# Kernel optimization log

Measured on AMD Instinct MI355X. Metric: run time of the kernel, lower is better.

Reference implementation:

```python
import jax, jax.numpy as jnp
import numpy as np

B, T, D = 8, 2048, 256
EPS_NORM = 1e-8
EPS_LN = 1e-6


def _layer_norm(x, gamma, beta):
    mu = jnp.mean(x, axis=-1, keepdims=True)
    var = jnp.var(x, axis=-1, keepdims=True)
    return (x - mu) * jax.lax.rsqrt(var + EPS_LN) * gamma + beta


def setup_inputs() -> dict:
    key = jax.random.key(0)
    ks = jax.random.split(key, 8)
    xav = np.sqrt(2.0 / (D + D)).astype(np.float32)  # xavier_uniform-ish scale
    a_fea = jax.random.normal(ks[0], (B, T, D), jnp.float32)
    v_fea = jax.random.normal(ks[1], (B, T, D), jnp.float32)
    Wv1 = jax.random.normal(ks[2], (D, D), jnp.float32) * xav
    Wv2 = jax.random.normal(ks[3], (D, D), jnp.float32) * xav
    Wa1 = jax.random.normal(ks[4], (D, D), jnp.float32) * xav
    Wa2 = jax.random.normal(ks[5], (D, D), jnp.float32) * xav
    ln_gamma = jnp.ones((D,), jnp.float32)
    ln_beta = jnp.zeros((D,), jnp.float32)
    thr_val = jnp.asarray(0.099, jnp.float32)
    return {"a_fea": a_fea, "v_fea": v_fea, "Wv1": Wv1, "Wv2": Wv2,
            "Wa1": Wa1, "Wa2": Wa2, "ln_gamma": ln_gamma, "ln_beta": ln_beta,
            "thr_val": thr_val}


def reference(a_fea, v_fea, Wv1, Wv2, Wa1, Wa2, ln_gamma, ln_beta, thr_val):
    # Dropout is identity in eval mode. Linear(bias=False): x @ W^T; here W is [in, out].
    v_b1 = jax.nn.relu(jnp.einsum('btd,dh->bth', v_fea, Wv1))
    v_b2 = jax.nn.relu(jnp.einsum('btd,dh->bth', v_fea, Wv2))
    a_b1 = jax.nn.relu(jnp.einsum('btd,dh->bth', a_fea, Wa1))
    a_b2 = jax.nn.relu(jnp.einsum('btd,dh->bth', a_fea, Wa2))

    scale = 1.0 / jnp.sqrt(jnp.asarray(v_b2.shape[2], jnp.float32))
    # relu-gated cross-modal scores [B, Tv, Ta]
    beta = jax.nn.relu(jnp.einsum('bvh,bah->bva', v_b2, a_b1) * scale)

    # v->a: normalize over audio axis, threshold-sparsify
    beta_va = beta / (jnp.sum(beta, axis=-1, keepdims=True) + EPS_NORM)
    gamma_va = jnp.where(beta_va > thr_val, beta_va, 0.0)
    # a->v: transpose of UN-normalized beta (faithful to source ordering)
    beta_av = jnp.swapaxes(beta, 1, 2)
    beta_av = beta_av / (jnp.sum(beta_av, axis=-1, keepdims=True) + EPS_NORM)
    gamma_av = jnp.where(beta_av > thr_val, beta_av, 0.0)

    a_pos = jnp.einsum('bva,bah->bvh', gamma_va, a_b2)
    v_pos = jnp.einsum('bav,bvh->bah', gamma_av, v_b1)

    v_psp = _layer_norm(v_fea + a_pos, ln_gamma, ln_beta)
    a_psp = _layer_norm(a_fea + v_pos, ln_gamma, ln_beta)
    return (v_psp + a_psp) * 0.5
```

## Files before the change

kernel.cpp:

```cpp
#include <hip/hip_runtime.h>
#include <stdint.h>

#define B_ 8
#define T_ 2048
#define D_ 256
#define M_ (B_*T_)

typedef uint16_t u16;
typedef __attribute__((ext_vector_type(8))) short   short8;
typedef __attribute__((ext_vector_type(8))) __bf16  bf16x8;
typedef __attribute__((ext_vector_type(4))) float   f32x4;

__device__ __forceinline__ float bf2f(u16 b){
    union { uint32_t u; float f; } v; v.u = ((uint32_t)b) << 16; return v.f;
}
__device__ __forceinline__ u16 f2bf(float f){
    union { float f; uint32_t u; } v; v.f = f;
    uint32_t u = v.u;
    u += 0x7FFFu + ((u >> 16) & 1u);
    return (u16)(u >> 16);
}

__global__ void k_detect(const uint32_t* g, int* flag){
    *flag = (g[0] == 0x3F803F80u) ? 0 : 1;
}

struct WtArgs { const void* w[4]; u16* wt[4]; const int* flag; };

__global__ __launch_bounds__(256) void k_wt(WtArgs a){
    int f32in = *a.flag;
    int m = blockIdx.y;
    int d = blockIdx.x;
    int h = threadIdx.x;
    float val;
    if (f32in) val = ((const float*)a.w[m])[(size_t)d * D_ + h];
    else       val = bf2f(((const u16*)a.w[m])[(size_t)d * D_ + h]);
    a.wt[m][(size_t)h * D_ + d] = f2bf(val);
}

struct ProjArgs { const void* x[4]; const u16* wt[4]; u16* y[4]; u16* yt[4]; const int* flag; };

__global__ __launch_bounds__(256) void k_proj(ProjArgs args){
    __shared__ __align__(16) u16 Xs[128][72];
    __shared__ __align__(16) u16 Ws[128][72];
    int f32in = *args.flag;
    int id = blockIdx.x;
    int m  = id & 127;
    int vh = id >> 7;
    int hh = vh & 1;
    int v  = vh >> 1;
    const u16* Wt = args.wt[v];
    u16*       Y  = args.y[v];
    u16*       YT = args.yt[v];
    int t_base = m * 128;
    int h_base = hh * 128;

    int tid  = threadIdx.x;
    int w    = tid >> 6, lane = tid & 63;
    int wm   = w >> 1, wn = w & 1;
    int l15  = lane & 15, quad = lane >> 4;

    int srow = tid >> 1;
    int shalf = tid & 1;

    f32x4 acc[4][4];
#pragma unroll
    for (int i = 0; i < 4; ++i)
#pragma unroll
        for (int j = 0; j < 4; ++j) acc[i][j] = (f32x4){0.f,0.f,0.f,0.f};

    float4 pXf[8];
    short8 pXb[4];
    short8 pW[4];

    const float* Xf = (const float*)args.x[v] + (size_t)(t_base + srow)*D_ + shalf*32;
    const u16*   Xb = (const u16*)args.x[v]   + (size_t)(t_base + srow)*D_ + shalf*32;
    const u16*   Wp = Wt + (size_t)(h_base + srow)*D_ + shalf*32;

    if (f32in){
#pragma unroll
        for (int i = 0; i < 8; ++i) pXf[i] = *(const float4*)(Xf + i*4);
    } else {
#pragma unroll
        for (int i = 0; i < 4; ++i) pXb[i] = *(const short8*)(Xb + i*8);
    }
#pragma unroll
    for (int i = 0; i < 4; ++i) pW[i] = *(const short8*)(Wp + i*8);

    for (int k0 = 0; k0 < D_; k0 += 64){
        __syncthreads();
        if (f32in){
#pragma unroll
            for (int i = 0; i < 4; ++i){
                float4 a0 = pXf[i*2], a1 = pXf[i*2+1];
                short8 o;
                o[0]=(short)f2bf(a0.x); o[1]=(short)f2bf(a0.y); o[2]=(short)f2bf(a0.z); o[3]=(short)f2bf(a0.w);
                o[4]=(short)f2bf(a1.x); o[5]=(short)f2bf(a1.y); o[6]=(short)f2bf(a1.z); o[7]=(short)f2bf(a1.w);
                *(short8*)(&Xs[srow][shalf*32 + i*8]) = o;
            }
        } else {
#pragma unroll
            for (int i = 0; i < 4; ++i) *(short8*)(&Xs[srow][shalf*32 + i*8]) = pXb[i];
        }
#pragma unroll
        for (int i = 0; i < 4; ++i) *(short8*)(&Ws[srow][shalf*32 + i*8]) = pW[i];

        int kn = k0 + 64;
        if (kn < D_){
            if (f32in){
#pragma unroll
                for (int i = 0; i < 8; ++i) pXf[i] = *(const float4*)(Xf + kn + i*4);
            } else {
#pragma unroll
                for (int i = 0; i < 4; ++i) pXb[i] = *(const short8*)(Xb + kn + i*8);
            }
#pragma unroll
            for (int i = 0; i < 4; ++i) pW[i] = *(const short8*)(Wp + kn + i*8);
        }
        __syncthreads();

#pragma unroll
        for (int kc = 0; kc < 2; ++kc){
            bf16x8 af[4], bf[4];
#pragma unroll
            for (int i = 0; i < 4; ++i){
                af[i] = __builtin_bit_cast(bf16x8,
                         *(const short8*)(&Xs[wm*64 + i*16 + l15][kc*32 + quad*8]));
                bf[i] = __builtin_bit_cast(bf16x8,
                         *(const short8*)(&Ws[wn*64 + i*16 + l15][kc*32 + quad*8]));
            }
#pragma unroll
            for (int mt = 0; mt < 4; ++mt)
#pragma unroll
                for (int nt = 0; nt < 4; ++nt)
                    acc[mt][nt] = __builtin_amdgcn_mfma_f32_16x16x32_bf16(
                                      af[mt], bf[nt], acc[mt][nt], 0, 0, 0);
        }
    }

    int v0 = t_base + wm*64;
    int h0 = h_base + wn*64;
#pragma unroll
    for (int mt = 0; mt < 4; ++mt){
#pragma unroll
        for (int nt = 0; nt < 4; ++nt){
            int col = h0 + nt*16 + l15;
            u16 q[4];
#pragma unroll
            for (int r = 0; r < 4; ++r){
                float s = acc[mt][nt][r]; s = s > 0.f ? s : 0.f;
                q[r] = f2bf(s);
            }
            if (Y){
#pragma unroll
                for (int r = 0; r < 4; ++r)
                    Y[(size_t)(v0 + mt*16 + quad*4 + r)*D_ + col] = q[r];
            }
            if (YT){
                uint2 pk;
                pk.x = (uint32_t)q[0] | ((uint32_t)q[1] << 16);
                pk.y = (uint32_t)q[2] | ((uint32_t)q[3] << 16);
                *(uint2*)(YT + (size_t)col*T_ + v0 + mt*16 + quad*4) = pk;
            }
        }
    }
}

__global__ __launch_bounds__(256) void k_score(const u16* vb2, const u16* ab1,
                                               u16* beta, float* rowsum, float* colsum){
    __shared__ __align__(16) u16 As[128][72];
    __shared__ __align__(16) u16 Bs[128][72];
    int id = blockIdx.x;
    int b  = id & 7;
    int t  = id >> 3;
    int mb = t & 15;
    int ab = t >> 4;
    int tid  = threadIdx.x;
    int w    = tid >> 6, lane = tid & 63;
    int wm   = w >> 1, wn = w & 1;
    int l15  = lane & 15, quad = lane >> 4;
    int v_base = mb*128;
    int a_base = ab*128;

    const u16* vb = vb2 + (size_t)b*T_*D_;
    const u16* an = ab1 + (size_t)b*T_*D_;
    u16*   bbp = beta + (size_t)b*T_*T_;
    float* rs  = rowsum + b*T_;
    float* cs  = colsum + b*T_;

    int kk = tid & 7;
    int mm = tid >> 3;

    f32x4 acc[4][4];
#pragma unroll
    for (int i = 0; i < 4; ++i)
#pragma unroll
        for (int j = 0; j < 4; ++j) acc[i][j] = (f32x4){0.f,0.f,0.f,0.f};

    short8 pA[4], pB[4];
#pragma unroll
    for (int i = 0; i < 4; ++i){
        int row = mm + i*32;
        pA[i] = *(const short8*)(vb + (size_t)(v_base + row)*D_ + kk*8);
        pB[i] = *(const short8*)(an + (size_t)(a_base + row)*D_ + kk*8);
    }

    for (int k0 = 0; k0 < D_; k0 += 64){
        __syncthreads();
#pragma unroll
        for (int i = 0; i < 4; ++i){
            int row = mm + i*32;
            *(short8*)(&As[row][kk*8]) = pA[i];
            *(short8*)(&Bs[row][kk*8]) = pB[i];
        }
        int kn = k0 + 64;
        if (kn < D_){
#pragma unroll
            for (int i = 0; i < 4; ++i){
                int row = mm + i*32;
                pA[i] = *(const short8*)(vb + (size_t)(v_base + row)*D_ + kn + kk*8);
                pB[i] = *(const short8*)(an + (size_t)(a_base + row)*D_ + kn + kk*8);
            }
        }
        __syncthreads();

#pragma unroll
        for (int kc = 0; kc < 2; ++kc){
            bf16x8 af[4], bf[4];
#pragma unroll
            for (int i = 0; i < 4; ++i){
                af[i] = __builtin_bit_cast(bf16x8,
                         *(const short8*)(&As[wm*64 + i*16 + l15][kc*32 + quad*8]));
                bf[i] = __builtin_bit_cast(bf16x8,
                         *(const short8*)(&Bs[wn*64 + i*16 + l15][kc*32 + quad*8]));
            }
#pragma unroll
            for (int mt = 0; mt < 4; ++mt)
#pragma unroll
                for (int nt = 0; nt < 4; ++nt)
                    acc[mt][nt] = __builtin_amdgcn_mfma_f32_16x16x32_bf16(
                                      af[mt], bf[nt], acc[mt][nt], 0, 0, 0);
        }
    }

    int v0 = v_base + wm*64;
    int a0 = a_base + wn*64;
    float rsum[4][4];
    float csum[4] = {0.f,0.f,0.f,0.f};
#pragma unroll
    for (int mt = 0; mt < 4; ++mt)
#pragma unroll
        for (int r = 0; r < 4; ++r) rsum[mt][r] = 0.f;

#pragma unroll
    for (int mt = 0; mt < 4; ++mt){
#pragma unroll
        for (int nt = 0; nt < 4; ++nt){
#pragma unroll
            for (int r = 0; r < 4; ++r){
                float s = acc[mt][nt][r] * 0.0625f;
                s = s > 0.f ? s : 0.f;
                bbp[(size_t)(v0 + mt*16 + quad*4 + r)*T_ + a0 + nt*16 + l15] = f2bf(s);
                rsum[mt][r] += s;
                csum[nt]    += s;
            }
        }
    }
#pragma unroll
    for (int mt = 0; mt < 4; ++mt){
#pragma unroll
        for (int r = 0; r < 4; ++r){
            float v = rsum[mt][r];
            v += __shfl_xor(v, 1);
            v += __shfl_xor(v, 2);
            v += __shfl_xor(v, 4);
            v += __shfl_xor(v, 8);
            if (l15 == 0) atomicAdd(&rs[v0 + mt*16 + quad*4 + r], v);
        }
    }
#pragma unroll
    for (int nt = 0; nt < 4; ++nt){
        float v = csum[nt];
        v += __shfl_xor(v, 16);
        v += __shfl_xor(v, 32);
        if (quad == 0) atomicAdd(&cs[a0 + nt*16 + l15], v);
    }
}

__global__ __launch_bounds__(256) void k_pos2(const u16* beta, const u16* ab2T, const u16* vb1T,
                                              const float* rowsum, const float* colsum,
                                              const void* thrp, const int* flag,
                                              u16* apos, u16* vpos){
    __shared__ __align__(16) u16 B2t[128][72];
    __shared__ __align__(16) u16 At[64][72];
    int f32in = *flag;
    int id    = blockIdx.x;
    int b     = id & 7;
    int nhalf = (id >> 3) & 1;
    int rest  = id >> 4;
    int mb    = rest & 31;
    int which = rest >> 5;
    int n0    = nhalf * 128;

    const u16* betab = beta + (size_t)b*T_*T_;
    const u16* B2T   = (which ? vb1T : ab2T) + (size_t)b*T_*D_;
    const float* nrm = (which ? colsum : rowsum) + b*T_;
    u16*       outb  = (which ? vpos : apos) + (size_t)b*T_*D_;

    int tid  = threadIdx.x;
    int wave = tid >> 6, lane = tid & 63;
    int l15  = lane & 15, quad = lane >> 4;
    int m_lane = mb*64 + wave*16 + l15;

    float inv = 1.f / (nrm[m_lane] + 1e-8f);
    float thr = f32in ? *(const float*)thrp : bf2f(*(const u16*)thrp);

    f32x4 acc[8];
#pragma unroll
    for (int i = 0; i < 8; ++i) acc[i] = (f32x4){0.f,0.f,0.f,0.f};

    short8 pv[4];
    short8 pa2[2];
    short8 araw[2];

#pragma unroll
    for (int i = 0; i < 4; ++i){
        int chunk = tid + i*256;
        int kk = chunk & 7, hh = chunk >> 3;
        pv[i] = *(const short8*)(B2T + (size_t)(n0 + hh)*T_ + kk*8);
    }
    if (which){
#pragma unroll
        for (int i = 0; i < 2; ++i){
            int chunk = tid + i*256;
            int kr = chunk & 63, mg = chunk >> 6;
            pa2[i] = *(const short8*)(betab + (size_t)kr*T_ + mb*64 + mg*8);
        }
    } else {
#pragma unroll
        for (int kc = 0; kc < 2; ++kc)
            araw[kc] = *(const short8*)(betab + (size_t)m_lane*T_ + kc*32 + quad*8);
    }

    for (int k0 = 0; k0 < T_; k0 += 64){
        __syncthreads();
#pragma unroll
        for (int i = 0; i < 4; ++i){
            int chunk = tid + i*256;
            int kk = chunk & 7, hh = chunk >> 3;
            *(short8*)(&B2t[hh][kk*8]) = pv[i];
        }
        short8 a_cur[2];
        if (which){
#pragma unroll
            for (int i = 0; i < 2; ++i){
                int chunk = tid + i*256;
                int kr = chunk & 63, mg = chunk >> 6;
                short8 d = pa2[i];
#pragma unroll
                for (int j = 0; j < 8; ++j) At[mg*8 + j][kr] = (u16)(short)d[j];
            }
        } else {
            a_cur[0] = araw[0]; a_cur[1] = araw[1];
        }
        int kn = k0 + 64;
        if (kn < T_){
#pragma unroll
            for (int i = 0; i < 4; ++i){
                int chunk = tid + i*256;
                int kk = chunk & 7, hh = chunk >> 3;
                pv[i] = *(const short8*)(B2T + (size_t)(n0 + hh)*T_ + kn + kk*8);
            }
            if (which){
#pragma unroll
                for (int i = 0; i < 2; ++i){
                    int chunk = tid + i*256;
                    int kr = chunk & 63, mg = chunk >> 6;
                    pa2[i] = *(const short8*)(betab + (size_t)(kn + kr)*T_ + mb*64 + mg*8);
                }
            } else {
#pragma unroll
                for (int kc = 0; kc < 2; ++kc)
                    araw[kc] = *(const short8*)(betab + (size_t)m_lane*T_ + kn + kc*32 + quad*8);
            }
        }
        __syncthreads();

        bf16x8 af[2];
#pragma unroll
        for (int kc = 0; kc < 2; ++kc){
            short8 raw;
            if (which) raw = *(const short8*)(&At[wave*16 + l15][kc*32 + quad*8]);
            else       raw = a_cur[kc];
            bf16x8 o;
#pragma unroll
            for (int j = 0; j < 8; ++j){
                float f = bf2f((u16)(short)raw[j]);
                float p = f * inv;
                p = (p > thr) ? p : 0.f;
                o[j] = (__bf16)p;
            }
            af[kc] = o;
        }
#pragma unroll
        for (int nt = 0; nt < 8; ++nt){
#pragma unroll
            for (int kc = 0; kc < 2; ++kc){
                short8 bfr = *(const short8*)(&B2t[nt*16 + l15][kc*32 + quad*8]);
                acc[nt] = __builtin_amdgcn_mfma_f32_16x16x32_bf16(
                              af[kc], __builtin_bit_cast(bf16x8, bfr), acc[nt], 0, 0, 0);
            }
        }
    }
#pragma unroll
    for (int nt = 0; nt < 8; ++nt)
#pragma unroll
        for (int r = 0; r < 4; ++r)
            outb[(size_t)(mb*64 + wave*16 + quad*4 + r)*D_ + n0 + nt*16 + l15] = f2bf(acc[nt][r]);
}

__global__ __launch_bounds__(256) void k_ln(const void* vfea, const void* afea,
                                            const u16* apos, const u16* vpos,
                                            const void* g, const void* lnb,
                                            const int* flag, void* out){
    int f32in = *flag;
    int row = blockIdx.x;
    int c   = threadIdx.x;
    size_t idx = (size_t)row * D_ + c;
    float xv = f32in ? ((const float*)vfea)[idx] : bf2f(((const u16*)vfea)[idx]);
    float xa = f32in ? ((const float*)afea)[idx] : bf2f(((const u16*)afea)[idx]);
    float x1 = xv + bf2f(apos[idx]);
    float x2 = xa + bf2f(vpos[idx]);
    float s1 = x1, q1 = x1*x1, s2 = x2, q2 = x2*x2;
#pragma unroll
    for (int off = 1; off < 64; off <<= 1){
        s1 += __shfl_xor(s1, off);
        q1 += __shfl_xor(q1, off);
        s2 += __shfl_xor(s2, off);
        q2 += __shfl_xor(q2, off);
    }
    __shared__ float red[4][4];
    int wave = threadIdx.x >> 6;
    if ((threadIdx.x & 63) == 0){
        red[0][wave] = s1; red[1][wave] = q1; red[2][wave] = s2; red[3][wave] = q2;
    }
    __syncthreads();
    s1 = red[0][0]+red[0][1]+red[0][2]+red[0][3];
    q1 = red[1][0]+red[1][1]+red[1][2]+red[1][3];
    s2 = red[2][0]+red[2][1]+red[2][2]+red[2][3];
    q2 = red[3][0]+red[3][1]+red[3][2]+red[3][3];
    const float invD = 1.f / (float)D_;
    float mu1 = s1*invD, mu2 = s2*invD;
    float var1 = q1*invD - mu1*mu1;
    float var2 = q2*invD - mu2*mu2;
    float rs1 = rsqrtf(var1 + 1e-6f);
    float rs2 = rsqrtf(var2 + 1e-6f);
    float gg = f32in ? ((const float*)g)[c]   : bf2f(((const u16*)g)[c]);
    float bv = f32in ? ((const float*)lnb)[c] : bf2f(((const u16*)lnb)[c]);
    float y = 0.5f * (((x1-mu1)*rs1)*gg + bv + ((x2-mu2)*rs2)*gg + bv);
    if (f32in) ((float*)out)[idx] = y;
    else       ((u16*)out)[idx]   = f2bf(y);
}

extern "C" void kernel_launch(void* const* d_in, const int* in_sizes, int n_in,
                              void* d_out, int out_size, void* d_ws, size_t ws_size,
                              hipStream_t stream){
    (void)in_sizes; (void)n_in; (void)out_size; (void)ws_size;
    const void* a_fea = d_in[0];
    const void* v_fea = d_in[1];
    const void* Wv1   = d_in[2];
    const void* Wv2   = d_in[3];
    const void* Wa1   = d_in[4];
    const void* Wa2   = d_in[5];
    const void* lng   = d_in[6];
    const void* lnb   = d_in[7];
    const void* thrp  = d_in[8];
    char* ws = (char*)d_ws;

    const size_t ACT = (size_t)M_ * D_ * 2;
    size_t off_wt    = 0;
    size_t off_vb1   = 524288;
    size_t off_vb2   = off_vb1  + ACT;
    size_t off_ab1   = off_vb2  + ACT;
    size_t off_ab2   = off_ab1  + ACT;
    size_t off_vb1T  = off_ab2  + ACT;
    size_t off_ab2T  = off_vb1T + ACT;
    size_t off_beta  = off_ab2T + ACT;
    size_t off_rsum  = off_beta + (size_t)B_*T_*T_*2;
    size_t off_csum  = off_rsum + (size_t)B_*T_*4;
    size_t off_apos  = off_csum + (size_t)B_*T_*4;
    size_t off_vpos  = off_apos + ACT;
    size_t off_flag  = off_vpos + ACT;

    u16* wt0  = (u16*)(ws + off_wt);
    u16* vb2  = (u16*)(ws + off_vb2);
    u16* ab1  = (u16*)(ws + off_ab1);
    u16* vb1T = (u16*)(ws + off_vb1T);
    u16* ab2T = (u16*)(ws + off_ab2T);
    u16* beta = (u16*)(ws + off_beta);
    float* rowsum = (float*)(ws + off_rsum);
    float* colsum = (float*)(ws + off_csum);
    u16*   apos   = (u16*)(ws + off_apos);
    u16*   vpos   = (u16*)(ws + off_vpos);
    int*   flag   = (int*)(ws + off_flag);

    hipMemsetAsync(ws + off_rsum, 0, 2 * (size_t)B_ * T_ * sizeof(float), stream);

    k_detect<<<1, 1, 0, stream>>>((const uint32_t*)lng, flag);

    WtArgs wa;
    wa.w[0] = Wv1; wa.w[1] = Wv2; wa.w[2] = Wa1; wa.w[3] = Wa2;
    for (int i = 0; i < 4; ++i) wa.wt[i] = wt0 + (size_t)i * D_ * D_;
    wa.flag = flag;
    k_wt<<<dim3(256,4), 256, 0, stream>>>(wa);

    ProjArgs pa;
    pa.x[0] = v_fea; pa.x[1] = v_fea; pa.x[2] = a_fea; pa.x[3] = a_fea;
    for (int i = 0; i < 4; ++i) pa.wt[i] = wa.wt[i];
    pa.y[0] = nullptr; pa.y[1] = vb2; pa.y[2] = ab1; pa.y[3] = nullptr;
    pa.yt[0] = vb1T;   pa.yt[1] = nullptr; pa.yt[2] = nullptr; pa.yt[3] = ab2T;
    pa.flag = flag;
    k_proj<<<4*2*(M_/128), 256, 0, stream>>>(pa);

    k_score<<<8*16*16, 256, 0, stream>>>(vb2, ab1, beta, rowsum, colsum);

    k_pos2<<<1024, 256, 0, stream>>>(beta, ab2T, vb1T, rowsum, colsum,
                                     thrp, flag, apos, vpos);

    k_ln<<<M_, 256, 0, stream>>>(v_fea, a_fea, apos, vpos, lng, lnb, flag, d_out);
}
```

Baseline: 248.8 us.

## Write transposed beta in score kernel and retile pos GEMM with async LDS loads

```diff
diff --git a/kernel.cpp b/kernel.cpp
--- a/kernel.cpp
+++ b/kernel.cpp
@@ -19,6 +19,12 @@
     uint32_t u = v.u;
     u += 0x7FFFu + ((u >> 16) & 1u);
     return (u16)(u >> 16);
+}
+
+typedef __attribute__((address_space(1))) void gvoid;
+typedef __attribute__((address_space(3))) void lvoid;
+__device__ __forceinline__ void gl16(const void* g, void* l){
+    __builtin_amdgcn_global_load_lds((gvoid*)(unsigned long long)g, (lvoid*)l, 16, 0, 0);
 }
 
 __global__ void k_detect(const uint32_t* g, int* flag){
@@ -157,17 +163,21 @@
                     Y[(size_t)(v0 + mt*16 + quad*4 + r)*D_ + col] = q[r];
             }
             if (YT){
+                int row0 = v0 + mt*16 + quad*4;
+                int bb   = row0 >> 11;
+                int tl   = row0 & (T_-1);
                 uint2 pk;
                 pk.x = (uint32_t)q[0] | ((uint32_t)q[1] << 16);
                 pk.y = (uint32_t)q[2] | ((uint32_t)q[3] << 16);
-                *(uint2*)(YT + (size_t)col*T_ + v0 + mt*16 + quad*4) = pk;
+                *(uint2*)(YT + ((size_t)(bb*D_ + col))*T_ + tl) = pk;
             }
         }
     }
 }
 
 __global__ __launch_bounds__(256) void k_score(const u16* vb2, const u16* ab1,
-                                               u16* beta, float* rowsum, float* colsum){
+                                               u16* beta, u16* betaT,
+                                               float* rowsum, float* colsum){
     __shared__ __align__(16) u16 As[128][72];
     __shared__ __align__(16) u16 Bs[128][72];
     int id = blockIdx.x;
@@ -184,7 +194,8 @@
 
     const u16* vb = vb2 + (size_t)b*T_*D_;
     const u16* an = ab1 + (size_t)b*T_*D_;
-    u16*   bbp = beta + (size_t)b*T_*T_;
+    u16*   bbp = beta  + (size_t)b*T_*T_;
+    u16*   bbt = betaT + (size_t)b*T_*T_;
     float* rs  = rowsum + b*T_;
     float* cs  = colsum + b*T_;
 
@@ -256,14 +267,20 @@
     for (int mt = 0; mt < 4; ++mt){
 #pragma unroll
         for (int nt = 0; nt < 4; ++nt){
+            u16 q[4];
 #pragma unroll
             for (int r = 0; r < 4; ++r){
                 float s = acc[mt][nt][r] * 0.0625f;
                 s = s > 0.f ? s : 0.f;
-                bbp[(size_t)(v0 + mt*16 + quad*4 + r)*T_ + a0 + nt*16 + l15] = f2bf(s);
+                q[r] = f2bf(s);
+                bbp[(size_t)(v0 + mt*16 + quad*4 + r)*T_ + a0 + nt*16 + l15] = q[r];
                 rsum[mt][r] += s;
                 csum[nt]    += s;
             }
+            uint2 pk;
+            pk.x = (uint32_t)q[0] | ((uint32_t)q[1] << 16);
+            pk.y = (uint32_t)q[2] | ((uint32_t)q[3] << 16);
+            *(uint2*)(bbt + (size_t)(a0 + nt*16 + l15)*T_ + v0 + mt*16 + quad*4) = pk;
         }
     }
 #pragma unroll
@@ -287,136 +304,108 @@
     }
 }
 
-__global__ __launch_bounds__(256) void k_pos2(const u16* beta, const u16* ab2T, const u16* vb1T,
+__global__ __launch_bounds__(256) void k_pos3(const u16* beta, const u16* betaT,
+                                              const u16* ab2T, const u16* vb1T,
                                               const float* rowsum, const float* colsum,
                                               const void* thrp, const int* flag,
                                               u16* apos, u16* vpos){
-    __shared__ __align__(16) u16 B2t[128][72];
-    __shared__ __align__(16) u16 At[64][72];
+    __shared__ __align__(16) u16 SL[2][2][128*64];
     int f32in = *flag;
-    int id    = blockIdx.x;
-    int b     = id & 7;
-    int nhalf = (id >> 3) & 1;
-    int rest  = id >> 4;
-    int mb    = rest & 31;
-    int which = rest >> 5;
-    int n0    = nhalf * 128;
-
-    const u16* betab = beta + (size_t)b*T_*T_;
-    const u16* B2T   = (which ? vb1T : ab2T) + (size_t)b*T_*D_;
+    int id = blockIdx.x;
+    int nb    = id & 1;
+    int mb    = (id >> 1) & 15;
+    int b     = (id >> 5) & 7;
+    int which = id >> 8;
+
+    const u16* A   = (which ? betaT : beta) + (size_t)b*T_*T_;
+    const u16* Bt  = (which ? vb1T  : ab2T) + (size_t)b*T_*D_;
     const float* nrm = (which ? colsum : rowsum) + b*T_;
-    u16*       outb  = (which ? vpos : apos) + (size_t)b*T_*D_;
-
-    int tid  = threadIdx.x;
-    int wave = tid >> 6, lane = tid & 63;
-    int l15  = lane & 15, quad = lane >> 4;
-    int m_lane = mb*64 + wave*16 + l15;
-
-    float inv = 1.f / (nrm[m_lane] + 1e-8f);
+    u16* outb = (which ? vpos : apos) + (size_t)b*T_*D_;
+
     float thr = f32in ? *(const float*)thrp : bf2f(*(const u16*)thrp);
 
-    f32x4 acc[8];
-#pragma unroll
-    for (int i = 0; i < 8; ++i) acc[i] = (f32x4){0.f,0.f,0.f,0.f};
-
-    short8 pv[4];
-    short8 pa2[2];
-    short8 araw[2];
-
-#pragma unroll
-    for (int i = 0; i < 4; ++i){
-        int chunk = tid + i*256;
-        int kk = chunk & 7, hh = chunk >> 3;
-        pv[i] = *(const short8*)(B2T + (size_t)(n0 + hh)*T_ + kk*8);
-    }
-    if (which){
-#pragma unroll
-        for (int i = 0; i < 2; ++i){
-            int chunk = tid + i*256;
-            int kr = chunk & 63, mg = chunk >> 6;
-            pa2[i] = *(const short8*)(betab + (size_t)kr*T_ + mb*64 + mg*8);
-        }
-    } else {
-#pragma unroll
-        for (int kc = 0; kc < 2; ++kc)
-            araw[kc] = *(const short8*)(betab + (size_t)m_lane*T_ + kc*32 + quad*8);
-    }
-
+    int tid = threadIdx.x;
+    int w = tid >> 6, lane = tid & 63;
+    int wm = w >> 1, wn = w & 1;
+    int l15 = lane & 15, quad = lane >> 4;
+
+    int m0 = mb * 128;
+    int h0 = nb * 128;
+
+    int srow = w*32 + (lane >> 3);
+    int schk = (lane & 7) ^ ((lane >> 3) & 7);
+    const u16* gA = A  + (size_t)(m0 + srow)*T_ + schk*8;
+    const u16* gB = Bt + (size_t)(h0 + srow)*T_ + schk*8;
+
+    float thra[4];
+#pragma unroll
+    for (int i = 0; i < 4; ++i)
+        thra[i] = thr * (nrm[m0 + wm*64 + i*16 + l15] + 1e-8f);
+
+    f32x4 acc[4][4];
+#pragma unroll
+    for (int i = 0; i < 4; ++i)
+#pragma unroll
+        for (int j = 0; j < 4; ++j) acc[i][j] = (f32x4){0.f,0.f,0.f,0.f};
+
+#pragma unroll
+    for (int c = 0; c < 4; ++c){
+        gl16(gA + (size_t)c*8*T_, &SL[0][0][(w*32 + c*8)*64]);
+        gl16(gB + (size_t)c*8*T_, &SL[0][1][(w*32 + c*8)*64]);
+    }
+
+    int q = 0;
     for (int k0 = 0; k0 < T_; k0 += 64){
         __syncthreads();
-#pragma unroll
-        for (int i = 0; i < 4; ++i){
-            int chunk = tid + i*256;
-            int kk = chunk & 7, hh = chunk >> 3;
-            *(short8*)(&B2t[hh][kk*8]) = pv[i];
-        }
-        short8 a_cur[2];
-        if (which){
-#pragma unroll
-            for (int i = 0; i < 2; ++i){
-                int chunk = tid + i*256;
-                int kr = chunk & 63, mg = chunk >> 6;
-                short8 d = pa2[i];
-#pragma unroll
-                for (int j = 0; j < 8; ++j) At[mg*8 + j][kr] = (u16)(short)d[j];
-            }
-        } else {
-            a_cur[0] = araw[0]; a_cur[1] = araw[1];
-        }
         int kn = k0 + 64;
         if (kn < T_){
 #pragma unroll
+            for (int c = 0; c < 4; ++c){
+                gl16(gA + (size_t)c*8*T_ + kn, &SL[q^1][0][(w*32 + c*8)*64]);
+                gl16(gB + (size_t)c*8*T_ + kn, &SL[q^1][1][(w*32 + c*8)*64]);
+            }
+        }
+        const u16* Asb = &SL[q][0][0];
+        const u16* Bsb = &SL[q][1][0];
+#pragma unroll
+        for (int kc = 0; kc < 2; ++kc){
+            int sw = ((kc*4 + quad) ^ (l15 & 7)) * 8;
+            bf16x8 af[4], bfr[4];
+#pragma unroll
             for (int i = 0; i < 4; ++i){
-                int chunk = tid + i*256;
-                int kk = chunk & 7, hh = chunk >> 3;
-                pv[i] = *(const short8*)(B2T + (size_t)(n0 + hh)*T_ + kn + kk*8);
-            }
-            if (which){
-#pragma unroll
-                for (int i = 0; i < 2; ++i){
-                    int chunk = tid + i*256;
-                    int kr = chunk & 63, mg = chunk >> 6;
-                    pa2[i] = *(const short8*)(betab + (size_t)(kn + kr)*T_ + mb*64 + mg*8);
+                short8 ra = *(const short8*)(Asb + (size_t)(wm*64 + i*16 + l15)*64 + sw);
+                short8 o;
+#pragma unroll
+                for (int j = 0; j < 8; ++j){
+                    u16 e = (u16)(short)ra[j];
+                    o[j] = (bf2f(e) > thra[i]) ? ra[j] : (short)0;
                 }
-            } else {
-#pragma unroll
-                for (int kc = 0; kc < 2; ++kc)
-                    araw[kc] = *(const short8*)(betab + (size_t)m_lane*T_ + kn + kc*32 + quad*8);
-            }
-        }
-        __syncthreads();
-
-        bf16x8 af[2];
-#pragma unroll
-        for (int kc = 0; kc < 2; ++kc){
-            short8 raw;
-            if (which) raw = *(const short8*)(&At[wave*16 + l15][kc*32 + quad*8]);
-            else       raw = a_cur[kc];
-            bf16x8 o;
-#pragma unroll
-            for (int j = 0; j < 8; ++j){
-                float f = bf2f((u16)(short)raw[j]);
-                float p = f * inv;
-                p = (p > thr) ? p : 0.f;
-                o[j] = (__bf16)p;
-            }
-            af[kc] = o;
-        }
-#pragma unroll
-        for (int nt = 0; nt < 8; ++nt){
-#pragma unroll
-            for (int kc = 0; kc < 2; ++kc){
-                short8 bfr = *(const short8*)(&B2t[nt*16 + l15][kc*32 + quad*8]);
-                acc[nt] = __builtin_amdgcn_mfma_f32_16x16x32_bf16(
-                              af[kc], __builtin_bit_cast(bf16x8, bfr), acc[nt], 0, 0, 0);
-            }
-        }
-    }
-#pragma unroll
-    for (int nt = 0; nt < 8; ++nt)
-#pragma unroll
-        for (int r = 0; r < 4; ++r)
-            outb[(size_t)(mb*64 + wave*16 + quad*4 + r)*D_ + n0 + nt*16 + l15] = f2bf(acc[nt][r]);
+                af[i]  = __builtin_bit_cast(bf16x8, o);
+                bfr[i] = __builtin_bit_cast(bf16x8,
+                          *(const short8*)(Bsb + (size_t)(wn*64 + i*16 + l15)*64 + sw));
+            }
+#pragma unroll
+            for (int mt = 0; mt < 4; ++mt)
+#pragma unroll
+                for (int nt = 0; nt < 4; ++nt)
+                    acc[mt][nt] = __builtin_amdgcn_mfma_f32_16x16x32_bf16(
+                                      af[mt], bfr[nt], acc[mt][nt], 0, 0, 0);
+        }
+        q ^= 1;
+    }
+
+#pragma unroll
+    for (int mt = 0; mt < 4; ++mt){
+#pragma unroll
+        for (int r = 0; r < 4; ++r){
+            int row = m0 + wm*64 + mt*16 + quad*4 + r;
+            float iv = 1.f / (nrm[row] + 1e-8f);
+#pragma unroll
+            for (int nt = 0; nt < 4; ++nt)
+                outb[(size_t)row*D_ + h0 + wn*64 + nt*16 + l15] =
+                    f2bf(acc[mt][nt][r] * iv);
+        }
+    }
 }
 
 __global__ __launch_bounds__(256) void k_ln(const void* vfea, const void* afea,
@@ -477,27 +466,28 @@
     const void* thrp  = d_in[8];
     char* ws = (char*)d_ws;
 
-    const size_t ACT = (size_t)M_ * D_ * 2;
+    const size_t ACT  = (size_t)M_ * D_ * 2;
+    const size_t BETA = (size_t)B_ * T_ * T_ * 2;
     size_t off_wt    = 0;
-    size_t off_vb1   = 524288;
-    size_t off_vb2   = off_vb1  + ACT;
+    size_t off_vb2   = 524288;
     size_t off_ab1   = off_vb2  + ACT;
-    size_t off_ab2   = off_ab1  + ACT;
-    size_t off_vb1T  = off_ab2  + ACT;
+    size_t off_vb1T  = off_ab1  + ACT;
     size_t off_ab2T  = off_vb1T + ACT;
     size_t off_beta  = off_ab2T + ACT;
-    size_t off_rsum  = off_beta + (size_t)B_*T_*T_*2;
+    size_t off_betaT = off_beta  + BETA;
+    size_t off_rsum  = off_betaT + BETA;
     size_t off_csum  = off_rsum + (size_t)B_*T_*4;
     size_t off_apos  = off_csum + (size_t)B_*T_*4;
     size_t off_vpos  = off_apos + ACT;
     size_t off_flag  = off_vpos + ACT;
 
-    u16* wt0  = (u16*)(ws + off_wt);
-    u16* vb2  = (u16*)(ws + off_vb2);
-    u16* ab1  = (u16*)(ws + off_ab1);
-    u16* vb1T = (u16*)(ws + off_vb1T);
-    u16* ab2T = (u16*)(ws + off_ab2T);
-    u16* beta = (u16*)(ws + off_beta);
+    u16* wt0   = (u16*)(ws + off_wt);
+    u16* vb2   = (u16*)(ws + off_vb2);
+    u16* ab1   = (u16*)(ws + off_ab1);
+    u16* vb1T  = (u16*)(ws + off_vb1T);
+    u16* ab2T  = (u16*)(ws + off_ab2T);
+    u16* beta  = (u16*)(ws + off_beta);
+    u16* betaT = (u16*)(ws + off_betaT);
     float* rowsum = (float*)(ws + off_rsum);
     float* colsum = (float*)(ws + off_csum);
     u16*   apos   = (u16*)(ws + off_apos);
@@ -522,10 +512,10 @@
     pa.flag = flag;
     k_proj<<<4*2*(M_/128), 256, 0, stream>>>(pa);
 
-    k_score<<<8*16*16, 256, 0, stream>>>(vb2, ab1, beta, rowsum, colsum);
-
-    k_pos2<<<1024, 256, 0, stream>>>(beta, ab2T, vb1T, rowsum, colsum,
-                                     thrp, flag, apos, vpos);
+    k_score<<<8*16*16, 256, 0, stream>>>(vb2, ab1, beta, betaT, rowsum, colsum);
+
+    k_pos3<<<512, 256, 0, stream>>>(beta, betaT, ab2T, vb1T, rowsum, colsum,
+                                    thrp, flag, apos, vpos);
 
     k_ln<<<M_, 256, 0, stream>>>(v_fea, a_fea, apos, vpos, lng, lnb, flag, d_out);
 }
```

After: 251.3 us. No clear change (+1.0%).
